# Optimization experiments

Hardware: AMD Instinct MI355X
Metric: run time of the kernel (lower is better)

## Reference

```python
import jax, jax.numpy as jnp
import numpy as np


def setup_inputs() -> dict:
    key = jax.random.key(0)
    k1, k2, k3 = jax.random.split(key, 3)
    B, T, C = 16, 8192, 256
    inputs = jax.random.normal(k1, (B, T, C), dtype=jnp.float32)
    initial_state = jax.random.normal(k2, (B, C), dtype=jnp.float32)
    # learned smoothing coeff, per-channel, init'd near coeff_init=0.1
    smooth = jax.random.uniform(k3, (C,), dtype=jnp.float32)
    return {"inputs": inputs, "initial_state": initial_state, "smooth": smooth}


def reference(inputs, initial_state, smooth):
    """EMA recurrence y_t = w*x_t + (1-w)*y_{t-1}, vectorized via associative scan.

    inputs: [B, T, C], initial_state: [B, C], smooth: [C].
    The linear recurrence y_t = a*y_{t-1} + b_t (a = 1-w, b_t = w*x_t) is
    computed in O(log T) depth with lax.associative_scan over pairs (a, b),
    composing (a1,b1) then (a2,b2) -> (a1*a2, a2*b1 + b2). The initial state
    is folded in afterwards: y_t = A_t * y_0 + B_t.
    """
    w = jnp.clip(smooth, 0.0, 1.0)                      # [C]
    a = jnp.broadcast_to(1.0 - w, inputs.shape)         # [B, T, C]
    b = w * inputs                                      # [B, T, C]

    def combine(c1, c2):
        a1, b1 = c1
        a2, b2 = c2
        return a1 * a2, a2 * b1 + b2

    A, Bc = jax.lax.associative_scan(combine, (a, b), axis=1)
    return A * initial_state[:, None, :] + Bc           # [B, T, C]
```

## Files before the change

kernel.cpp:

```cpp
#include <hip/hip_runtime.h>


#define CHUNK_L 64

__device__ __forceinline__ float clip01(float v) {
    return fminf(fmaxf(v, 0.0f), 1.0f);
}

__global__ __launch_bounds__(64) void ema_k1_chunk_last(
    const float* __restrict__ x, const float* __restrict__ smooth,
    float* __restrict__ chunk_last, int T, int C, int P) {
    const int blk = blockIdx.x;
    const int b = blk / P;
    const int p = blk - b * P;
    const int c = threadIdx.x << 2;

    float4 w4 = *(const float4*)(smooth + c);
    w4.x = clip01(w4.x); w4.y = clip01(w4.y); w4.z = clip01(w4.z); w4.w = clip01(w4.w);
    const float ax = 1.0f - w4.x, ay = 1.0f - w4.y, az = 1.0f - w4.z, aw = 1.0f - w4.w;

    const int sF4 = C >> 2;
    const float4* xp = (const float4*)(x + ((size_t)b * T + (size_t)p * CHUNK_L) * C) + threadIdx.x;

    float y0 = 0.0f, y1 = 0.0f, y2 = 0.0f, y3 = 0.0f;
    for (int i0 = 0; i0 < CHUNK_L; i0 += 8) {
        float4 xv[8];
#pragma unroll
        for (int j = 0; j < 8; ++j) xv[j] = xp[(size_t)(i0 + j) * sF4];
#pragma unroll
        for (int j = 0; j < 8; ++j) {
            y0 = fmaf(ax, y0, w4.x * xv[j].x);
            y1 = fmaf(ay, y1, w4.y * xv[j].y);
            y2 = fmaf(az, y2, w4.z * xv[j].z);
            y3 = fmaf(aw, y3, w4.w * xv[j].w);
        }
    }
    float4 r; r.x = y0; r.y = y1; r.z = y2; r.w = y3;
    *(float4*)(chunk_last + (size_t)blk * C + c) = r;
}

__global__ __launch_bounds__(64) void ema_k2_apply(
    const float* __restrict__ x, const float* __restrict__ smooth,
    const float* __restrict__ chunk_last, const float* __restrict__ init,
    float* __restrict__ out, int T, int C, int P) {
    const int blk = blockIdx.x;
    const int b = blk / P;
    const int p = blk - b * P;
    const int c = threadIdx.x << 2;

    float4 w4 = *(const float4*)(smooth + c);
    w4.x = clip01(w4.x); w4.y = clip01(w4.y); w4.z = clip01(w4.z); w4.w = clip01(w4.w);
    const float ax = 1.0f - w4.x, ay = 1.0f - w4.y, az = 1.0f - w4.z, aw = 1.0f - w4.w;

    float aLx = ax, aLy = ay, aLz = az, aLw = aw;
    for (int e = CHUNK_L; e > 1; e >>= 1) { aLx *= aLx; aLy *= aLy; aLz *= aLz; aLw *= aLw; }

    float4 s = *(const float4*)(init + (size_t)b * C + c);
    const float* cl = chunk_last + (size_t)b * P * C + c;
    int q = 0;
    for (; q + 8 <= p; q += 8) {
        float4 l[8];
#pragma unroll
        for (int j = 0; j < 8; ++j) l[j] = *(const float4*)(cl + (size_t)(q + j) * C);
#pragma unroll
        for (int j = 0; j < 8; ++j) {
            s.x = fmaf(aLx, s.x, l[j].x);
            s.y = fmaf(aLy, s.y, l[j].y);
            s.z = fmaf(aLz, s.z, l[j].z);
            s.w = fmaf(aLw, s.w, l[j].w);
        }
    }
    for (; q < p; ++q) {
        float4 l = *(const float4*)(cl + (size_t)q * C);
        s.x = fmaf(aLx, s.x, l.x);
        s.y = fmaf(aLy, s.y, l.y);
        s.z = fmaf(aLz, s.z, l.z);
        s.w = fmaf(aLw, s.w, l.w);
    }

    const int sF4 = C >> 2;
    const size_t base = ((size_t)b * T + (size_t)p * CHUNK_L) * C;
    const float4* xp = (const float4*)(x + base) + threadIdx.x;
    float4* op = (float4*)(out + base) + threadIdx.x;

    float y0 = s.x, y1 = s.y, y2 = s.z, y3 = s.w;
    for (int i0 = 0; i0 < CHUNK_L; i0 += 8) {
        float4 xv[8];
#pragma unroll
        for (int j = 0; j < 8; ++j) xv[j] = xp[(size_t)(i0 + j) * sF4];
#pragma unroll
        for (int j = 0; j < 8; ++j) {
            y0 = fmaf(ax, y0, w4.x * xv[j].x);
            y1 = fmaf(ay, y1, w4.y * xv[j].y);
            y2 = fmaf(az, y2, w4.z * xv[j].z);
            y3 = fmaf(aw, y3, w4.w * xv[j].w);
            float4 r; r.x = y0; r.y = y1; r.z = y2; r.w = y3;
            op[(size_t)(i0 + j) * sF4] = r;
        }
    }
}

extern "C" void kernel_launch(void* const* d_in, const int* in_sizes, int n_in,
                              void* d_out, int out_size, void* d_ws, size_t ws_size,
                              hipStream_t stream) {
    const float* x      = (const float*)d_in[0];
    const float* init   = (const float*)d_in[1];
    const float* smooth = (const float*)d_in[2];
    float* out = (float*)d_out;

    const int C  = in_sizes[2];
    const int BC = in_sizes[1];
    const int B  = BC / C;
    const int T  = in_sizes[0] / BC;
    const int P  = T / CHUNK_L;

    float* chunk_last = (float*)d_ws;

    ema_k1_chunk_last<<<dim3(B * P), dim3(C / 4), 0, stream>>>(x, smooth, chunk_last, T, C, P);
    ema_k2_apply<<<dim3(B * P), dim3(C / 4), 0, stream>>>(x, smooth, chunk_last, init, out, T, C, P);
}
```

Measured before the change: 272.0 us.

## Fuse chunk-summary and apply kernels into one with flag-based chunk handoff

Merges the two EMA kernels into a single kernel. Each block publishes its chunk's last value to a workspace with a release flag, then spins with acquire loads on the flags of all earlier chunks in its batch row before building its carry-in state. It then re-scans its own chunk to write outputs, so the second read of x can come from cache rather than a separate kernel pass, and one launch boundary is removed. The cost is an extra memset of the flags and spin-waiting that depends on earlier blocks being resident and making progress.

```diff
diff --git a/kernel.cpp b/kernel.cpp
--- a/kernel.cpp
+++ b/kernel.cpp
@@ -7,9 +7,11 @@
     return fminf(fmaxf(v, 0.0f), 1.0f);
 }
 
-__global__ __launch_bounds__(64) void ema_k1_chunk_last(
+__global__ __launch_bounds__(64) void ema_fused(
     const float* __restrict__ x, const float* __restrict__ smooth,
-    float* __restrict__ chunk_last, int T, int C, int P) {
+    const float* __restrict__ init, float* __restrict__ out,
+    float* __restrict__ chunk_last, unsigned int* __restrict__ flags,
+    int T, int C, int P) {
     const int blk = blockIdx.x;
     const int b = blk / P;
     const int p = blk - b * P;
@@ -20,7 +22,8 @@
     const float ax = 1.0f - w4.x, ay = 1.0f - w4.y, az = 1.0f - w4.z, aw = 1.0f - w4.w;
 
     const int sF4 = C >> 2;
-    const float4* xp = (const float4*)(x + ((size_t)b * T + (size_t)p * CHUNK_L) * C) + threadIdx.x;
+    const size_t base = ((size_t)b * T + (size_t)p * CHUNK_L) * C;
+    const float4* xp = (const float4*)(x + base) + threadIdx.x;
 
     float y0 = 0.0f, y1 = 0.0f, y2 = 0.0f, y3 = 0.0f;
     for (int i0 = 0; i0 < CHUNK_L; i0 += 8) {
@@ -35,30 +38,28 @@
             y3 = fmaf(aw, y3, w4.w * xv[j].w);
         }
     }
-    float4 r; r.x = y0; r.y = y1; r.z = y2; r.w = y3;
-    *(float4*)(chunk_last + (size_t)blk * C + c) = r;
-}
-
-__global__ __launch_bounds__(64) void ema_k2_apply(
-    const float* __restrict__ x, const float* __restrict__ smooth,
-    const float* __restrict__ chunk_last, const float* __restrict__ init,
-    float* __restrict__ out, int T, int C, int P) {
-    const int blk = blockIdx.x;
-    const int b = blk / P;
-    const int p = blk - b * P;
-    const int c = threadIdx.x << 2;
-
-    float4 w4 = *(const float4*)(smooth + c);
-    w4.x = clip01(w4.x); w4.y = clip01(w4.y); w4.z = clip01(w4.z); w4.w = clip01(w4.w);
-    const float ax = 1.0f - w4.x, ay = 1.0f - w4.y, az = 1.0f - w4.z, aw = 1.0f - w4.w;
+    {
+        float4 r; r.x = y0; r.y = y1; r.z = y2; r.w = y3;
+        *(float4*)(chunk_last + (size_t)blk * C + c) = r;
+    }
+    if (threadIdx.x == 0) {
+        __hip_atomic_store(flags + blk, 1u, __ATOMIC_RELEASE, __HIP_MEMORY_SCOPE_AGENT);
+    }
 
     float aLx = ax, aLy = ay, aLz = az, aLw = aw;
     for (int e = CHUNK_L; e > 1; e >>= 1) { aLx *= aLx; aLy *= aLy; aLz *= aLz; aLw *= aLw; }
 
     float4 s = *(const float4*)(init + (size_t)b * C + c);
     const float* cl = chunk_last + (size_t)b * P * C + c;
+    const unsigned int* fl = flags + (size_t)b * P;
     int q = 0;
     for (; q + 8 <= p; q += 8) {
+        if (threadIdx.x < 8) {
+            while (__hip_atomic_load(fl + q + threadIdx.x, __ATOMIC_ACQUIRE,
+                                     __HIP_MEMORY_SCOPE_AGENT) == 0u) {
+                __builtin_amdgcn_s_sleep(1);
+            }
+        }
         float4 l[8];
 #pragma unroll
         for (int j = 0; j < 8; ++j) l[j] = *(const float4*)(cl + (size_t)(q + j) * C);
@@ -71,6 +72,10 @@
         }
     }
     for (; q < p; ++q) {
+        while (__hip_atomic_load(fl + q, __ATOMIC_ACQUIRE,
+                                 __HIP_MEMORY_SCOPE_AGENT) == 0u) {
+            __builtin_amdgcn_s_sleep(1);
+        }
         float4 l = *(const float4*)(cl + (size_t)q * C);
         s.x = fmaf(aLx, s.x, l.x);
         s.y = fmaf(aLy, s.y, l.y);
@@ -78,23 +83,19 @@
         s.w = fmaf(aLw, s.w, l.w);
     }
 
-    const int sF4 = C >> 2;
-    const size_t base = ((size_t)b * T + (size_t)p * CHUNK_L) * C;
-    const float4* xp = (const float4*)(x + base) + threadIdx.x;
     float4* op = (float4*)(out + base) + threadIdx.x;
-
-    float y0 = s.x, y1 = s.y, y2 = s.z, y3 = s.w;
+    float yb0 = s.x, yb1 = s.y, yb2 = s.z, yb3 = s.w;
     for (int i0 = 0; i0 < CHUNK_L; i0 += 8) {
         float4 xv[8];
 #pragma unroll
         for (int j = 0; j < 8; ++j) xv[j] = xp[(size_t)(i0 + j) * sF4];
 #pragma unroll
         for (int j = 0; j < 8; ++j) {
-            y0 = fmaf(ax, y0, w4.x * xv[j].x);
-            y1 = fmaf(ay, y1, w4.y * xv[j].y);
-            y2 = fmaf(az, y2, w4.z * xv[j].z);
-            y3 = fmaf(aw, y3, w4.w * xv[j].w);
-            float4 r; r.x = y0; r.y = y1; r.z = y2; r.w = y3;
+            yb0 = fmaf(ax, yb0, w4.x * xv[j].x);
+            yb1 = fmaf(ay, yb1, w4.y * xv[j].y);
+            yb2 = fmaf(az, yb2, w4.z * xv[j].z);
+            yb3 = fmaf(aw, yb3, w4.w * xv[j].w);
+            float4 r; r.x = yb0; r.y = yb1; r.z = yb2; r.w = yb3;
             op[(size_t)(i0 + j) * sF4] = r;
         }
     }
@@ -115,7 +116,11 @@
     const int P  = T / CHUNK_L;
 
     float* chunk_last = (float*)d_ws;
+    unsigned int* flags =
+        (unsigned int*)((char*)d_ws + (size_t)B * P * C * sizeof(float));
 
-    ema_k1_chunk_last<<<dim3(B * P), dim3(C / 4), 0, stream>>>(x, smooth, chunk_last, T, C, P);
-    ema_k2_apply<<<dim3(B * P), dim3(C / 4), 0, stream>>>(x, smooth, chunk_last, init, out, T, C, P);
+    hipMemsetAsync(flags, 0, (size_t)B * P * sizeof(unsigned int), stream);
+
+    ema_fused<<<dim3(B * P), dim3(C / 4), 0, stream>>>(
+        x, smooth, init, out, chunk_last, flags, T, C, P);
 }
```

Result: slower. 523.4 us (+92.5%).
